# Kernel optimization log

Measured on AMD Instinct MI355X. Metric: run time of the kernel, lower is better.

Reference implementation:

```python
import jax, jax.numpy as jnp
import numpy as np

N_SRC1, N_DST1, N_DST2 = 200000, 50000, 10000
E1, E2 = 2000000, 400000
IN_F, H_F, N_CLS = 128, 256, 47


def setup_inputs() -> dict:
    key = jax.random.key(0)
    ks = jax.random.split(key, 10)
    x = jax.random.normal(ks[0], (N_SRC1, IN_F), dtype=jnp.float32)
    W_self1 = jax.random.normal(ks[1], (IN_F, H_F), dtype=jnp.float32) * (1.0 / np.sqrt(IN_F))
    W_neigh1 = jax.random.normal(ks[2], (IN_F, H_F), dtype=jnp.float32) * (1.0 / np.sqrt(IN_F))
    b1 = jnp.zeros((H_F,), dtype=jnp.float32)
    W_self2 = jax.random.normal(ks[3], (H_F, N_CLS), dtype=jnp.float32) * (1.0 / np.sqrt(H_F))
    W_neigh2 = jax.random.normal(ks[4], (H_F, N_CLS), dtype=jnp.float32) * (1.0 / np.sqrt(H_F))
    b2 = jnp.zeros((N_CLS,), dtype=jnp.float32)
    src1 = jax.random.randint(ks[5], (E1,), 0, N_SRC1, dtype=jnp.int64)
    dst1 = jnp.sort(jax.random.randint(ks[6], (E1,), 0, N_DST1, dtype=jnp.int64))
    src2 = jax.random.randint(ks[7], (E2,), 0, N_DST1, dtype=jnp.int64)
    dst2 = jnp.sort(jax.random.randint(ks[8], (E2,), 0, N_DST2, dtype=jnp.int64))
    return {"x": x, "W_self1": W_self1, "W_neigh1": W_neigh1, "b1": b1,
            "W_self2": W_self2, "W_neigh2": W_neigh2, "b2": b2,
            "src1": src1, "dst1": dst1, "src2": src2, "dst2": dst2,
            "n_dst1": N_DST1, "n_dst2": N_DST2}


def _sage_mean(h_src, h_dst, src, dst, n_dst, W_self, W_neigh, b):
    # mean neighbor aggregation: gather src feats, segment-sum onto dst, divide by in-degree
    msum = jax.ops.segment_sum(h_src[src], dst, num_segments=n_dst)  # [n_dst, F]
    deg = jax.ops.segment_sum(jnp.ones(src.shape, h_src.dtype), dst, num_segments=n_dst)
    h_neigh = msum / jnp.maximum(deg, 1.0)[:, None]
    return h_dst @ W_self + h_neigh @ W_neigh + b


def reference(x, W_self1, W_neigh1, b1, W_self2, W_neigh2, b2,
              src1, dst1, src2, dst2, n_dst1, n_dst2):
    # layer 1 (dst nodes are the prefix of src nodes, DGL MFG convention)
    h = _sage_mean(x, x[:n_dst1], src1, dst1, n_dst1, W_self1, W_neigh1, b1)
    h = jax.nn.relu(h)  # dropout = identity (eval mode)
    # layer 2
    out = _sage_mean(h, h[:n_dst2], src2, dst2, n_dst2, W_self2, W_neigh2, b2)
    return out
```

## Files before the change

### kernel.cpp

```cpp
#include <hip/hip_runtime.h>

constexpr int N_DST1 = 50000;
constexpr int N_DST2 = 10000;
constexpr int E1     = 2000000;
constexpr int E2     = 400000;
constexpr int IN_F   = 128;
constexpr int H_F    = 256;
constexpr int N_CLS  = 47;

constexpr size_t RP1_OFF = 0;
constexpr size_t RP2_OFF = 204800;
constexpr size_t BPS_OFF = 245760;
constexpr size_t BPN_OFF = 311296;
constexpr size_t BP2_OFF = 376832;
constexpr size_t X8_OFF  = 430080;
constexpr size_t HB_OFF  = 38830080;
constexpr size_t H8_OFF  = 64430080;

using f32x4  = __attribute__((ext_vector_type(4))) float;
using f32x2  = __attribute__((ext_vector_type(2))) float;
using short8 = __attribute__((ext_vector_type(8))) short;

__device__ __forceinline__ ushort f2bf(float f) {
    union { float f; unsigned u; } v; v.f = f;
    unsigned u = v.u;
    return (ushort)((u + 0x7fffu + ((u >> 16) & 1u)) >> 16);
}

constexpr int CAST_BLKS = 200000 * IN_F / 8 / 256;
constexpr int PACK_BLKS = 44;
constexpr int RP_BLKS   = (N_DST1 + N_DST2 + 2 + 255) / 256;

__global__ __launch_bounds__(256) void setup_all(
    const float* __restrict__ x, unsigned char* __restrict__ x8,
    const float* __restrict__ Ws1, const float* __restrict__ Wn1,
    const float* __restrict__ Ws2, const float* __restrict__ Wn2,
    ushort* __restrict__ bps, ushort* __restrict__ bpn, ushort* __restrict__ bp2,
    const int* __restrict__ dst1, const int* __restrict__ dst2,
    int* __restrict__ rp1, int* __restrict__ rp2) {
    int b = blockIdx.x;
    if (b < CAST_BLKS) {
        int i = b * 256 + threadIdx.x;
        float4 v0 = ((const float4*)x)[2 * i];
        float4 v1 = ((const float4*)x)[2 * i + 1];
        int p0 = __builtin_amdgcn_cvt_pk_fp8_f32(v0.x, v0.y, 0, false);
        p0     = __builtin_amdgcn_cvt_pk_fp8_f32(v0.z, v0.w, p0, true);
        int p1 = __builtin_amdgcn_cvt_pk_fp8_f32(v1.x, v1.y, 0, false);
        p1     = __builtin_amdgcn_cvt_pk_fp8_f32(v1.z, v1.w, p1, true);
        uint2 o; o.x = (unsigned)p0; o.y = (unsigned)p1;
        ((uint2*)x8)[i] = o;
    } else if (b < CAST_BLKS + PACK_BLKS) {
        int pb = b - CAST_BLKS;
        if (pb < 32) {
            const float* W = (pb < 16) ? Ws1 : Wn1;
            ushort* P      = (pb < 16) ? bps : bpn;
            int idx = (pb & 15) * 256 + threadIdx.x;
            int lane = idx & 63, kb = (idx >> 6) & 3, nb = idx >> 8;
            int n  = nb * 16 + (lane & 15);
            int k0 = kb * 32 + ((lane >> 4) * 8);
            ushort tmp[8];
#pragma unroll
            for (int j = 0; j < 8; ++j) tmp[j] = f2bf(W[(k0 + j) * H_F + n]);
            ((uint4*)P)[idx] = *(uint4*)tmp;
        } else {
            int idx = (pb - 32) * 256 + threadIdx.x;
            if (idx < 3072) {
                int lane = idx & 63, rem = idx >> 6;
                int nb = rem % 3, kb = rem / 3;
                int col = nb * 16 + (lane & 15);
                int k0  = (kb & 7) * 32 + ((lane >> 4) * 8);
                const float* W = (kb < 8) ? Ws2 : Wn2;
                ushort tmp[8];
#pragma unroll
                for (int j = 0; j < 8; ++j)
                    tmp[j] = (col < N_CLS) ? f2bf(W[(k0 + j) * N_CLS + col]) : (ushort)0;
                ((uint4*)bp2)[(kb * 3 + nb) * 64 + lane] = *(uint4*)tmp;
            }
        }
    } else {
        int idx = (b - CAST_BLKS - PACK_BLKS) * 256 + threadIdx.x;
        const int* dst; int* rp; int E; int target;
        if (idx <= N_DST1) { dst = dst1; rp = rp1; E = E1; target = idx; }
        else if (idx <= N_DST1 + 1 + N_DST2) {
            dst = dst2; rp = rp2; E = E2; target = idx - (N_DST1 + 1);
        } else return;
        int lo = 0, hi = E;
        while (lo < hi) {
            int mid = (lo + hi) >> 1;
            if (dst[mid] < target) lo = mid + 1; else hi = mid;
        }
        rp[target] = lo;
    }
}

__global__ __launch_bounds__(256, 4) void fused1(
    const unsigned char* __restrict__ x8, const int* __restrict__ src,
    const int* __restrict__ rp, const float* __restrict__ x,
    const ushort* __restrict__ BpS, const ushort* __restrict__ BpN,
    const float* __restrict__ b1, ushort* __restrict__ hb,
    unsigned char* __restrict__ h8) {
    __shared__ ushort lhn[16][136];
    int tid = threadIdx.x;
    int wave = tid >> 6, lane = tid & 63;
    int m0 = blockIdx.x * 16;

    const uint4* x4 = (const uint4*)x8;
    int g = lane >> 3, c = lane & 7;
#pragma unroll 1
    for (int q = 0; q < 4; ++q) {
        int row = wave * 4 + q;
        int d = m0 + row;
        int s = rp[d], e = rp[d + 1];
        int deg = e - s;
        float a[16] = {};
        auto acc16 = [&](uint4 v) {
            f32x2 f;
            f = __builtin_amdgcn_cvt_pk_f32_fp8((int)v.x, false); a[0]  += f[0]; a[1]  += f[1];
            f = __builtin_amdgcn_cvt_pk_f32_fp8((int)v.x, true);  a[2]  += f[0]; a[3]  += f[1];
            f = __builtin_amdgcn_cvt_pk_f32_fp8((int)v.y, false); a[4]  += f[0]; a[5]  += f[1];
            f = __builtin_amdgcn_cvt_pk_f32_fp8((int)v.y, true);  a[6]  += f[0]; a[7]  += f[1];
            f = __builtin_amdgcn_cvt_pk_f32_fp8((int)v.z, false); a[8]  += f[0]; a[9]  += f[1];
            f = __builtin_amdgcn_cvt_pk_f32_fp8((int)v.z, true);  a[10] += f[0]; a[11] += f[1];
            f = __builtin_amdgcn_cvt_pk_f32_fp8((int)v.w, false); a[12] += f[0]; a[13] += f[1];
            f = __builtin_amdgcn_cvt_pk_f32_fp8((int)v.w, true);  a[14] += f[0]; a[15] += f[1];
        };
        int nfull = deg >> 3;
        int j = 0;
        for (; j + 2 <= nfull; j += 2) {
            int e0 = src[s + 8 * j + g];
            int e1 = src[s + 8 * j + 8 + g];
            uint4 v0 = x4[(size_t)e0 * 8 + c];
            uint4 v1 = x4[(size_t)e1 * 8 + c];
            acc16(v0);
            acc16(v1);
        }
        for (; j < nfull; ++j) {
            int e0 = src[s + 8 * j + g];
            uint4 v = x4[(size_t)e0 * 8 + c];
            acc16(v);
        }
        int b0 = s + 8 * nfull;
        int n = e - b0;
        if (g < n) {
            int e0 = src[b0 + g];
            uint4 v = x4[(size_t)e0 * 8 + c];
            acc16(v);
        }
#pragma unroll
        for (int qq = 0; qq < 16; ++qq) {
            a[qq] += __shfl_xor(a[qq], 8);
            a[qq] += __shfl_xor(a[qq], 16);
            a[qq] += __shfl_xor(a[qq], 32);
        }
        if (lane < 8) {
            float inv = 1.f / fmaxf((float)deg, 1.f);
            unsigned o[8];
#pragma unroll
            for (int p = 0; p < 8; ++p)
                o[p] = (unsigned)f2bf(a[2 * p] * inv) |
                       ((unsigned)f2bf(a[2 * p + 1] * inv) << 16);
            uint4* dp = (uint4*)&lhn[row][lane * 16];
            dp[0] = make_uint4(o[0], o[1], o[2], o[3]);
            dp[1] = make_uint4(o[4], o[5], o[6], o[7]);
        }
    }
    __syncthreads();

    int nb0 = wave * 4;
    int mloc = lane & 15;
    int mrow = m0 + mloc;
    int koff = (lane >> 4) * 8;

    const float* Af = x + (size_t)mrow * IN_F;
    short8 a0[4], a1[4];
#pragma unroll
    for (int kb = 0; kb < 4; ++kb) {
        float4 q0 = *(const float4*)(Af + kb * 32 + koff);
        float4 q1 = *(const float4*)(Af + kb * 32 + koff + 4);
        a0[kb][0] = (short)f2bf(q0.x); a0[kb][1] = (short)f2bf(q0.y);
        a0[kb][2] = (short)f2bf(q0.z); a0[kb][3] = (short)f2bf(q0.w);
        a0[kb][4] = (short)f2bf(q1.x); a0[kb][5] = (short)f2bf(q1.y);
        a0[kb][6] = (short)f2bf(q1.z); a0[kb][7] = (short)f2bf(q1.w);
        a1[kb] = *(const short8*)&lhn[mloc][kb * 32 + koff];
    }

    f32x4 acc[4];
#pragma unroll
    for (int nb = 0; nb < 4; ++nb) acc[nb] = (f32x4){0.f, 0.f, 0.f, 0.f};

#pragma unroll
    for (int kb = 0; kb < 4; ++kb)
#pragma unroll
        for (int nb = 0; nb < 4; ++nb) {
            short8 b = *(const short8*)(BpS + ((size_t)((nb0 + nb) * 4 + kb) * 64 + lane) * 8);
            acc[nb] = __builtin_amdgcn_mfma_f32_16x16x32_bf16(a0[kb], b, acc[nb], 0, 0, 0);
        }
#pragma unroll
    for (int kb = 0; kb < 4; ++kb)
#pragma unroll
        for (int nb = 0; nb < 4; ++nb) {
            short8 b = *(const short8*)(BpN + ((size_t)((nb0 + nb) * 4 + kb) * 64 + lane) * 8);
            acc[nb] = __builtin_amdgcn_mfma_f32_16x16x32_bf16(a1[kb], b, acc[nb], 0, 0, 0);
        }

    int crow0 = m0 + (lane >> 4) * 4;
    int ccol  = lane & 15;
#pragma unroll
    for (int nb = 0; nb < 4; ++nb) {
        size_t col = (size_t)(nb0 + nb) * 16 + ccol;
        float bias = b1[col];
#pragma unroll
        for (int r = 0; r < 4; ++r) {
            int row = crow0 + r;
            float v = fmaxf(acc[nb][r] + bias, 0.f);
            int p = __builtin_amdgcn_cvt_pk_fp8_f32(v, v, 0, false);
            h8[(size_t)row * H_F + col] = (unsigned char)(p & 0xff);
            if (row < N_DST2) hb[(size_t)row * H_F + col] = f2bf(v);
        }
    }
}

__global__ __launch_bounds__(256, 4) void fused2(
    const unsigned char* __restrict__ h8, const int* __restrict__ src,
    const int* __restrict__ rp, const ushort* __restrict__ hb,
    const ushort* __restrict__ P2, const float* __restrict__ b2,
    float* __restrict__ out) {
    __shared__ ushort lhn[16][264];
    __shared__ float lred[3][3][64][4];
    int tid = threadIdx.x;
    int wave = tid >> 6, lane = tid & 63;
    int m0 = blockIdx.x * 16;

    const uint4* h4 = (const uint4*)h8;
    int g = lane >> 4, c = lane & 15;
#pragma unroll 1
    for (int q = 0; q < 4; ++q) {
        int row = wave * 4 + q;
        int d = m0 + row;
        int s = rp[d], e = rp[d + 1];
        int deg = e - s;
        float a[16] = {};
        auto acc16 = [&](uint4 v) {
            f32x2 f;
            f = __builtin_amdgcn_cvt_pk_f32_fp8((int)v.x, false); a[0]  += f[0]; a[1]  += f[1];
            f = __builtin_amdgcn_cvt_pk_f32_fp8((int)v.x, true);  a[2]  += f[0]; a[3]  += f[1];
            f = __builtin_amdgcn_cvt_pk_f32_fp8((int)v.y, false); a[4]  += f[0]; a[5]  += f[1];
            f = __builtin_amdgcn_cvt_pk_f32_fp8((int)v.y, true);  a[6]  += f[0]; a[7]  += f[1];
            f = __builtin_amdgcn_cvt_pk_f32_fp8((int)v.z, false); a[8]  += f[0]; a[9]  += f[1];
            f = __builtin_amdgcn_cvt_pk_f32_fp8((int)v.z, true);  a[10] += f[0]; a[11] += f[1];
            f = __builtin_amdgcn_cvt_pk_f32_fp8((int)v.w, false); a[12] += f[0]; a[13] += f[1];
            f = __builtin_amdgcn_cvt_pk_f32_fp8((int)v.w, true);  a[14] += f[0]; a[15] += f[1];
        };
        int nfull = deg >> 2;
        int j = 0;
        for (; j + 2 <= nfull; j += 2) {
            int e0 = src[s + 4 * j + g];
            int e1 = src[s + 4 * j + 4 + g];
            uint4 v0 = h4[(size_t)e0 * 16 + c];
            uint4 v1 = h4[(size_t)e1 * 16 + c];
            acc16(v0);
            acc16(v1);
        }
        for (; j < nfull; ++j) {
            int e0 = src[s + 4 * j + g];
            uint4 v = h4[(size_t)e0 * 16 + c];
            acc16(v);
        }
        int b0 = s + 4 * nfull;
        int n = e - b0;
        if (g < n) {
            int e0 = src[b0 + g];
            uint4 v = h4[(size_t)e0 * 16 + c];
            acc16(v);
        }
#pragma unroll
        for (int qq = 0; qq < 16; ++qq) {
            a[qq] += __shfl_xor(a[qq], 16);
            a[qq] += __shfl_xor(a[qq], 32);
        }
        if (lane < 16) {
            float inv = 1.f / fmaxf((float)deg, 1.f);
            unsigned o[8];
#pragma unroll
            for (int p = 0; p < 8; ++p)
                o[p] = (unsigned)f2bf(a[2 * p] * inv) |
                       ((unsigned)f2bf(a[2 * p + 1] * inv) << 16);
            uint4* dp = (uint4*)&lhn[row][lane * 16];
            dp[0] = make_uint4(o[0], o[1], o[2], o[3]);
            dp[1] = make_uint4(o[4], o[5], o[6], o[7]);
        }
    }
    __syncthreads();

    int mloc = lane & 15;
    int mrow = m0 + mloc;
    int koff = (lane >> 4) * 8;

    f32x4 acc[3];
#pragma unroll
    for (int nb = 0; nb < 3; ++nb) acc[nb] = (f32x4){0.f, 0.f, 0.f, 0.f};

#pragma unroll
    for (int i = 0; i < 4; ++i) {
        int kb = wave * 4 + i;
        short8 a;
        if (wave < 2)
            a = *(const short8*)(hb + (size_t)mrow * H_F + kb * 32 + koff);
        else
            a = *(const short8*)&lhn[mloc][(kb - 8) * 32 + koff];
#pragma unroll
        for (int nb = 0; nb < 3; ++nb) {
            short8 b = *(const short8*)(P2 + ((size_t)(kb * 3 + nb) * 64 + lane) * 8);
            acc[nb] = __builtin_amdgcn_mfma_f32_16x16x32_bf16(a, b, acc[nb], 0, 0, 0);
        }
    }

    if (wave != 0) {
#pragma unroll
        for (int nb = 0; nb < 3; ++nb)
#pragma unroll
            for (int r = 0; r < 4; ++r)
                lred[wave - 1][nb][lane][r] = acc[nb][r];
    }
    __syncthreads();
    if (wave == 0) {
        int crow0 = m0 + (lane >> 4) * 4;
        int ccol  = lane & 15;
#pragma unroll
        for (int nb = 0; nb < 3; ++nb) {
            int col = nb * 16 + ccol;
#pragma unroll
            for (int r = 0; r < 4; ++r)
                acc[nb][r] += lred[0][nb][lane][r] + lred[1][nb][lane][r] +
                              lred[2][nb][lane][r];
            if (col < N_CLS) {
                float bias = b2[col];
#pragma unroll
                for (int r = 0; r < 4; ++r)
                    out[(size_t)(crow0 + r) * N_CLS + col] = acc[nb][r] + bias;
            }
        }
    }
}

extern "C" void kernel_launch(void* const* d_in, const int* in_sizes, int n_in,
                              void* d_out, int out_size, void* d_ws, size_t ws_size,
                              hipStream_t stream) {
    const float* x   = (const float*)d_in[0];
    const float* Ws1 = (const float*)d_in[1];
    const float* Wn1 = (const float*)d_in[2];
    const float* b1  = (const float*)d_in[3];
    const float* Ws2 = (const float*)d_in[4];
    const float* Wn2 = (const float*)d_in[5];
    const float* b2  = (const float*)d_in[6];
    const int* src1  = (const int*)d_in[7];
    const int* dst1  = (const int*)d_in[8];
    const int* src2  = (const int*)d_in[9];
    const int* dst2  = (const int*)d_in[10];
    float* out = (float*)d_out;

    char* ws = (char*)d_ws;
    int*           rp1 = (int*)(ws + RP1_OFF);
    int*           rp2 = (int*)(ws + RP2_OFF);
    ushort*        bps = (ushort*)(ws + BPS_OFF);
    ushort*        bpn = (ushort*)(ws + BPN_OFF);
    ushort*        bp2 = (ushort*)(ws + BP2_OFF);
    unsigned char* x8  = (unsigned char*)(ws + X8_OFF);
    ushort*        hb  = (ushort*)(ws + HB_OFF);
    unsigned char* h8  = (unsigned char*)(ws + H8_OFF);

    setup_all<<<CAST_BLKS + PACK_BLKS + RP_BLKS, 256, 0, stream>>>(
        x, x8, Ws1, Wn1, Ws2, Wn2, bps, bpn, bp2, dst1, dst2, rp1, rp2);
    fused1<<<N_DST1 / 16, 256, 0, stream>>>(x8, src1, rp1, x, bps, bpn, b1, hb, h8);
    fused2<<<N_DST2 / 16, 256, 0, stream>>>(h8, src2, rp2, hb, bp2, b2, out);
}
```

Before: 310.9 us.

## Use 16 waves per block, one destination row per wave in both layers

Both fused kernels now launch 1024-thread blocks, so each of 16 waves aggregates a single destination row instead of four waves looping over four rows each. In layer 1 each wave then computes one 16-column output tile with the MFMA, where before each wave computed four. In layer 2 only the first four waves do the GEMM and the rest idle. The aim is more memory-level parallelism in the neighbor gather and less serial per-wave latency, at the cost of larger blocks that may limit occupancy and duplicate A-fragment loads across waves.

```diff
diff --git a/kernel.cpp b/kernel.cpp
--- a/kernel.cpp
+++ b/kernel.cpp
@@ -93,7 +93,7 @@
     }
 }
 
-__global__ __launch_bounds__(256, 4) void fused1(
+__global__ __launch_bounds__(1024, 8) void fused1(
     const unsigned char* __restrict__ x8, const int* __restrict__ src,
     const int* __restrict__ rp, const float* __restrict__ x,
     const ushort* __restrict__ BpS, const ushort* __restrict__ BpN,
@@ -104,12 +104,10 @@
     int wave = tid >> 6, lane = tid & 63;
     int m0 = blockIdx.x * 16;
 
-    const uint4* x4 = (const uint4*)x8;
-    int g = lane >> 3, c = lane & 7;
-#pragma unroll 1
-    for (int q = 0; q < 4; ++q) {
-        int row = wave * 4 + q;
-        int d = m0 + row;
+    {
+        const uint4* x4 = (const uint4*)x8;
+        int g = lane >> 3, c = lane & 7;
+        int d = m0 + wave;
         int s = rp[d], e = rp[d + 1];
         int deg = e - s;
         float a[16] = {};
@@ -159,14 +157,14 @@
             for (int p = 0; p < 8; ++p)
                 o[p] = (unsigned)f2bf(a[2 * p] * inv) |
                        ((unsigned)f2bf(a[2 * p + 1] * inv) << 16);
-            uint4* dp = (uint4*)&lhn[row][lane * 16];
+            uint4* dp = (uint4*)&lhn[wave][lane * 16];
             dp[0] = make_uint4(o[0], o[1], o[2], o[3]);
             dp[1] = make_uint4(o[4], o[5], o[6], o[7]);
         }
     }
     __syncthreads();
 
-    int nb0 = wave * 4;
+    int nb = wave;
     int mloc = lane & 15;
     int mrow = m0 + mloc;
     int koff = (lane >> 4) * 8;
@@ -184,35 +182,27 @@
         a1[kb] = *(const short8*)&lhn[mloc][kb * 32 + koff];
     }
 
-    f32x4 acc[4];
-#pragma unroll
-    for (int nb = 0; nb < 4; ++nb) acc[nb] = (f32x4){0.f, 0.f, 0.f, 0.f};
-
-#pragma unroll
-    for (int kb = 0; kb < 4; ++kb)
-#pragma unroll
-        for (int nb = 0; nb < 4; ++nb) {
-            short8 b = *(const short8*)(BpS + ((size_t)((nb0 + nb) * 4 + kb) * 64 + lane) * 8);
-            acc[nb] = __builtin_amdgcn_mfma_f32_16x16x32_bf16(a0[kb], b, acc[nb], 0, 0, 0);
-        }
-#pragma unroll
-    for (int kb = 0; kb < 4; ++kb)
-#pragma unroll
-        for (int nb = 0; nb < 4; ++nb) {
-            short8 b = *(const short8*)(BpN + ((size_t)((nb0 + nb) * 4 + kb) * 64 + lane) * 8);
-            acc[nb] = __builtin_amdgcn_mfma_f32_16x16x32_bf16(a1[kb], b, acc[nb], 0, 0, 0);
-        }
+    f32x4 acc = (f32x4){0.f, 0.f, 0.f, 0.f};
+#pragma unroll
+    for (int kb = 0; kb < 4; ++kb) {
+        short8 b = *(const short8*)(BpS + ((size_t)(nb * 4 + kb) * 64 + lane) * 8);
+        acc = __builtin_amdgcn_mfma_f32_16x16x32_bf16(a0[kb], b, acc, 0, 0, 0);
+    }
+#pragma unroll
+    for (int kb = 0; kb < 4; ++kb) {
+        short8 b = *(const short8*)(BpN + ((size_t)(nb * 4 + kb) * 64 + lane) * 8);
+        acc = __builtin_amdgcn_mfma_f32_16x16x32_bf16(a1[kb], b, acc, 0, 0, 0);
+    }
 
     int crow0 = m0 + (lane >> 4) * 4;
     int ccol  = lane & 15;
-#pragma unroll
-    for (int nb = 0; nb < 4; ++nb) {
-        size_t col = (size_t)(nb0 + nb) * 16 + ccol;
+    {
+        size_t col = (size_t)nb * 16 + ccol;
         float bias = b1[col];
 #pragma unroll
         for (int r = 0; r < 4; ++r) {
             int row = crow0 + r;
-            float v = fmaxf(acc[nb][r] + bias, 0.f);
+            float v = fmaxf(acc[r] + bias, 0.f);
             int p = __builtin_amdgcn_cvt_pk_fp8_f32(v, v, 0, false);
             h8[(size_t)row * H_F + col] = (unsigned char)(p & 0xff);
             if (row < N_DST2) hb[(size_t)row * H_F + col] = f2bf(v);
@@ -220,7 +210,7 @@
     }
 }
 
-__global__ __launch_bounds__(256, 4) void fused2(
+__global__ __launch_bounds__(1024, 8) void fused2(
     const unsigned char* __restrict__ h8, const int* __restrict__ src,
     const int* __restrict__ rp, const ushort* __restrict__ hb,
     const ushort* __restrict__ P2, const float* __restrict__ b2,
@@ -231,12 +221,10 @@
     int wave = tid >> 6, lane = tid & 63;
     int m0 = blockIdx.x * 16;
 
-    const uint4* h4 = (const uint4*)h8;
-    int g = lane >> 4, c = lane & 15;
-#pragma unroll 1
-    for (int q = 0; q < 4; ++q) {
-        int row = wave * 4 + q;
-        int d = m0 + row;
+    {
+        const uint4* h4 = (const uint4*)h8;
+        int g = lane >> 4, c = lane & 15;
+        int d = m0 + wave;
         int s = rp[d], e = rp[d + 1];
         int deg = e - s;
         float a[16] = {};
@@ -285,7 +273,7 @@
             for (int p = 0; p < 8; ++p)
                 o[p] = (unsigned)f2bf(a[2 * p] * inv) |
                        ((unsigned)f2bf(a[2 * p + 1] * inv) << 16);
-            uint4* dp = (uint4*)&lhn[row][lane * 16];
+            uint4* dp = (uint4*)&lhn[wave][lane * 16];
             dp[0] = make_uint4(o[0], o[1], o[2], o[3]);
             dp[1] = make_uint4(o[4], o[5], o[6], o[7]);
         }
@@ -298,46 +286,47 @@
 
     f32x4 acc[3];
 #pragma unroll
-    for (int nb = 0; nb < 3; ++nb) acc[nb] = (f32x4){0.f, 0.f, 0.f, 0.f};
-
-#pragma unroll
-    for (int i = 0; i < 4; ++i) {
-        int kb = wave * 4 + i;
-        short8 a;
-        if (wave < 2)
-            a = *(const short8*)(hb + (size_t)mrow * H_F + kb * 32 + koff);
-        else
-            a = *(const short8*)&lhn[mloc][(kb - 8) * 32 + koff];
-#pragma unroll
-        for (int nb = 0; nb < 3; ++nb) {
-            short8 b = *(const short8*)(P2 + ((size_t)(kb * 3 + nb) * 64 + lane) * 8);
-            acc[nb] = __builtin_amdgcn_mfma_f32_16x16x32_bf16(a, b, acc[nb], 0, 0, 0);
-        }
-    }
-
-    if (wave != 0) {
-#pragma unroll
-        for (int nb = 0; nb < 3; ++nb)
-#pragma unroll
-            for (int r = 0; r < 4; ++r)
-                lred[wave - 1][nb][lane][r] = acc[nb][r];
+    for (int nbq = 0; nbq < 3; ++nbq) acc[nbq] = (f32x4){0.f, 0.f, 0.f, 0.f};
+
+    if (wave < 4) {
+#pragma unroll
+        for (int i = 0; i < 4; ++i) {
+            int kb = wave * 4 + i;
+            short8 a;
+            if (wave < 2)
+                a = *(const short8*)(hb + (size_t)mrow * H_F + kb * 32 + koff);
+            else
+                a = *(const short8*)&lhn[mloc][(kb - 8) * 32 + koff];
+#pragma unroll
+            for (int nbq = 0; nbq < 3; ++nbq) {
+                short8 b = *(const short8*)(P2 + ((size_t)(kb * 3 + nbq) * 64 + lane) * 8);
+                acc[nbq] = __builtin_amdgcn_mfma_f32_16x16x32_bf16(a, b, acc[nbq], 0, 0, 0);
+            }
+        }
+        if (wave != 0) {
+#pragma unroll
+            for (int nbq = 0; nbq < 3; ++nbq)
+#pragma unroll
+                for (int r = 0; r < 4; ++r)
+                    lred[wave - 1][nbq][lane][r] = acc[nbq][r];
+        }
     }
     __syncthreads();
     if (wave == 0) {
         int crow0 = m0 + (lane >> 4) * 4;
         int ccol  = lane & 15;
 #pragma unroll
-        for (int nb = 0; nb < 3; ++nb) {
-            int col = nb * 16 + ccol;
+        for (int nbq = 0; nbq < 3; ++nbq) {
+            int col = nbq * 16 + ccol;
 #pragma unroll
             for (int r = 0; r < 4; ++r)
-                acc[nb][r] += lred[0][nb][lane][r] + lred[1][nb][lane][r] +
-                              lred[2][nb][lane][r];
+                acc[nbq][r] += lred[0][nbq][lane][r] + lred[1][nbq][lane][r] +
+                               lred[2][nbq][lane][r];
             if (col < N_CLS) {
                 float bias = b2[col];
 #pragma unroll
                 for (int r = 0; r < 4; ++r)
-                    out[(size_t)(crow0 + r) * N_CLS + col] = acc[nb][r] + bias;
+                    out[(size_t)(crow0 + r) * N_CLS + col] = acc[nbq][r] + bias;
             }
         }
     }
@@ -371,6 +360,6 @@
 
     setup_all<<<CAST_BLKS + PACK_BLKS + RP_BLKS, 256, 0, stream>>>(
         x, x8, Ws1, Wn1, Ws2, Wn2, bps, bpn, bp2, dst1, dst2, rp1, rp2);
-    fused1<<<N_DST1 / 16, 256, 0, stream>>>(x8, src1, rp1, x, bps, bpn, b1, hb, h8);
-    fused2<<<N_DST2 / 16, 256, 0, stream>>>(h8, src2, rp2, hb, bp2, b2, out);
-}
+    fused1<<<N_DST1 / 16, 1024, 0, stream>>>(x8, src1, rp1, x, bps, bpn, b1, hb, h8);
+    fused2<<<N_DST2 / 16, 1024, 0, stream>>>(h8, src2, rp2, hb, bp2, b2, out);
+}
```

New measurement: 327.2 us. 1.05x slower.
